# Kernel optimization log

Hardware: AMD Instinct MI355X
Metric: run time of the kernel (lower is better)

The kernel has to match this reference:

```python
import jax, jax.numpy as jnp
import numpy as np

SIGMA = 1.0  # kernel bandwidth (init kwarg)

VS = 4096   # src vertices
VT = 4096   # tar vertices
FS = 8192   # src triangles
FT = 8192   # tar triangles
FR = 8192   # reference triangles


def setup_inputs() -> dict:
    key = jax.random.key(0)
    k0, k1, k2, k3, k4, k5 = jax.random.split(key, 6)
    src_vertices = jax.random.normal(k0, (VS, 3), dtype=jnp.float32)
    src_indices = jax.random.randint(k1, (FS, 3), 0, VS, dtype=jnp.int64)
    tar_vertices = jax.random.normal(k2, (VT, 3), dtype=jnp.float32)
    tar_indices = jax.random.randint(k3, (FT, 3), 0, VT, dtype=jnp.int64)
    ref_normals = 0.1 * jax.random.normal(k4, (FR, 3), dtype=jnp.float32)
    ref_centers = jax.random.normal(k5, (FR, 3), dtype=jnp.float32)
    return {
        "src_vertices": src_vertices,
        "src_indices": src_indices,
        "tar_vertices": tar_vertices,
        "tar_indices": tar_indices,
        "ref_normals": ref_normals,
        "ref_centers": ref_centers,
    }


def _tri_normals_centers(vertices, indices):
    tris = vertices[indices]               # [F, 3, 3]
    a, b, c = tris[:, 0, :], tris[:, 1, :], tris[:, 2, :]
    normals = 0.5 * jnp.cross(a - b, c - b)  # [F, 3]
    centers = tris.sum(axis=1) / 3.0         # [F, 3]
    return normals, centers


def _sqdist(src, tar):
    # d[i, j] = ||tar_i - src_j||^2  -> shape [Nt, Ns]
    s2 = jnp.sum(src * src, axis=-1)  # [Ns]
    t2 = jnp.sum(tar * tar, axis=-1)  # [Nt]
    return t2[:, None] + s2[None, :] - 2.0 * (tar @ src.T)


def _cauchy(d):
    return 1.0 / (1.0 + d / SIGMA) ** 2


def _energy(sn, sc, tn, tc):
    e1 = jnp.sum((sn @ sn.T) * _cauchy(_sqdist(sc, sc)))
    e2 = jnp.sum((tn @ sn.T) * _cauchy(_sqdist(sc, tc)))
    e3 = jnp.sum((tn @ tn.T) * _cauchy(_sqdist(tc, tc)))
    return e1 - 2.0 * e2 + e3


def reference(src_vertices, src_indices, tar_vertices, tar_indices, ref_normals, ref_centers):
    src_n, src_c = _tri_normals_centers(src_vertices, src_indices)
    tar_n, tar_c = _tri_normals_centers(tar_vertices, tar_indices)
    energy = _energy(src_n, src_c, ref_normals, ref_centers)
    energy = energy + _energy(tar_n, tar_c, ref_normals, ref_centers)
    energy = energy + 0.8 * _energy(src_n, src_c, tar_n, tar_c)
    return energy
```

## Files before the change

kernel.cpp:

```cpp
#include <hip/hip_runtime.h>

#define NSEG 8192
#define NPTS (3 * NSEG)
#define NSUP 96
#define NXB  192
#define NYG  13

typedef short bf16x8 __attribute__((ext_vector_type(8)));
typedef float f32x16 __attribute__((ext_vector_type(16)));
typedef unsigned short u16;

__device__ __forceinline__ u16 f2bf(float x) {
    unsigned u = __builtin_bit_cast(unsigned, x);
    return (u16)((u + 0x7FFFu + ((u >> 16) & 1u)) >> 16);
}
__device__ __forceinline__ float bf2f(u16 h) {
    unsigned u = ((unsigned)h) << 16;
    return __builtin_bit_cast(float, u);
}

__device__ __forceinline__ void compute_point(
    int seg, int f,
    const float* __restrict__ sv, const int* __restrict__ si,
    const float* __restrict__ tv, const int* __restrict__ ti,
    const float* __restrict__ rn, const float* __restrict__ rc,
    float& cx, float& cy, float& cz, float& nx, float& ny, float& nz)
{
    if (seg == 2) {
        nx = rn[3*f];   ny = rn[3*f+1]; nz = rn[3*f+2];
        cx = rc[3*f];   cy = rc[3*f+1]; cz = rc[3*f+2];
    } else {
        const float* v  = (seg == 0) ? sv : tv;
        const int*   nd = (seg == 0) ? si : ti;
        int i0 = nd[3*f], i1 = nd[3*f+1], i2 = nd[3*f+2];
        float ax = v[3*i0], ay = v[3*i0+1], az = v[3*i0+2];
        float bx = v[3*i1], by = v[3*i1+1], bz = v[3*i1+2];
        float gx = v[3*i2], gy = v[3*i2+1], gz = v[3*i2+2];
        float ux = ax-bx, uy = ay-by, uz = az-bz;
        float wx = gx-bx, wy = gy-by, wz = gz-bz;
        nx = 0.5f*(uy*wz - uz*wy);
        ny = 0.5f*(uz*wx - ux*wz);
        nz = 0.5f*(ux*wy - uy*wx);
        cx = (ax+bx+gx)*(1.0f/3.0f);
        cy = (ay+by+gy)*(1.0f/3.0f);
        cz = (az+bz+gz)*(1.0f/3.0f);
    }
}

__global__ void setup_feats(const float* __restrict__ sv, const int* __restrict__ si,
                            const float* __restrict__ tv, const int* __restrict__ ti,
                            const float* __restrict__ rn, const float* __restrict__ rc,
                            u16* __restrict__ ws, float* __restrict__ out) {
    int gid = blockIdx.x * 256 + threadIdx.x;
    if (gid == 0) out[0] = 0.0f;
    const int rec = (gid >= NPTS);
    const int p   = rec ? gid - NPTS : gid;
    int seg = p >> 13, f = p & (NSEG - 1);
    float cx, cy, cz, nx, ny, nz;
    compute_point(seg, f, sv, si, tv, ti, rn, rc, cx, cy, cz, nx, ny, nz);

    const u16 ONE = 0x3F80;
    float s = cx*cx + cy*cy + cz*cz;
    u16 chx = f2bf(cx), chy = f2bf(cy), chz = f2bf(cz);
    u16 clx = f2bf(cx - bf2f(chx)), cly = f2bf(cy - bf2f(chy)), clz = f2bf(cz - bf2f(chz));
    u16 sh  = f2bf(s);
    u16 sl  = f2bf(s - bf2f(sh));
    u16 nhx = f2bf(nx), nhy = f2bf(ny), nhz = f2bf(nz);
    u16 nlx = f2bf(nx - bf2f(nhx)), nly = f2bf(ny - bf2f(nhy)), nlz = f2bf(nz - bf2f(nhz));

    bf16x8* A8 = (bf16x8*)ws;
    bf16x8* B8 = A8 + (size_t)NPTS*4;
    u16 r0[16], r1[16];
    if (!rec) {
        u16 at[16] = {chx,chy,chz, clx,cly,clz, chx,chy,chz, sh, sl, ONE, ONE, ONE, 0, 0};
        u16 an[16] = {nhx,nhy,nhz, nlx,nly,nlz, nhx,nhy,nhz, 0,0,0,0,0,0,0};
        #pragma unroll
        for (int k = 0; k < 16; ++k) { r0[k] = at[k]; r1[k] = an[k]; }
    } else {
        u16 m2hx = f2bf(-2.0f*bf2f(chx)), m2hy = f2bf(-2.0f*bf2f(chy)), m2hz = f2bf(-2.0f*bf2f(chz));
        u16 m2lx = f2bf(-2.0f*bf2f(clx)), m2ly = f2bf(-2.0f*bf2f(cly)), m2lz = f2bf(-2.0f*bf2f(clz));
        u16 bt[16] = {m2hx,m2hy,m2hz, m2hx,m2hy,m2hz, m2lx,m2ly,m2lz, ONE, ONE, sh, sl, ONE, 0, 0};
        u16 bn[16] = {nhx,nhy,nhz, nhx,nhy,nhz, nlx,nly,nlz, 0,0,0,0,0,0,0};
        #pragma unroll
        for (int k = 0; k < 16; ++k) { r0[k] = bt[k]; r1[k] = bn[k]; }
    }
    bf16x8* dst = rec ? B8 : A8;
    bf16x8 v0, v1, v2, v3;
    #pragma unroll
    for (int k = 0; k < 8; ++k) { v0[k] = (short)r0[k]; v1[k] = (short)r0[k+8];
                                  v2[k] = (short)r1[k]; v3[k] = (short)r1[k+8]; }
    dst[(size_t)p*4+0] = v0; dst[(size_t)p*4+1] = v1;
    dst[(size_t)p*4+2] = v2; dst[(size_t)p*4+3] = v3;
}

__device__ __forceinline__ void mfma2_vgpr(const bf16x8& a1, const bf16x8& b1,
                                           const bf16x8& a2, const bf16x8& b2,
                                           const f32x16& Z, f32x16& d1, f32x16& d2) {
    asm("v_mfma_f32_32x32x16_bf16 %0, %2, %3, %6\n\t"
        "v_mfma_f32_32x32x16_bf16 %1, %4, %5, %6\n\t"
        "s_nop 7\n\t"
        "s_nop 7\n\t"
        "s_nop 7"
        : "=&v"(d1), "=&v"(d2)
        : "v"(a1), "v"(b1), "v"(a2), "v"(b2), "v"(Z));
}

__launch_bounds__(256, 3)
__global__ void energy_mfma(const u16* __restrict__ ws, float* __restrict__ out) {
    const int tid  = threadIdx.x;
    const int lane = tid & 63, wid = tid >> 6;
    const int half = lane >> 5, r32 = lane & 31;

    const int bx = blockIdx.x;
    const int X  = bx >> 1;
    const int g  = blockIdx.y;
    const int y0   = (g < 12) ? 4*g : 48;
    const int ycnt = (g < 12) ? 4 : 1;
    const int gi = X >> 5;

    const float Wt[9] = {1.8f, -0.8f, -1.0f,
                        -0.8f,  1.8f, -1.0f,
                        -1.0f, -1.0f,  2.0f};

    const bf16x8* A8 = (const bf16x8*)ws;
    const bf16x8* B8 = A8 + (size_t)NPTS*4;

    const int pi = X*256 + (bx & 1)*128 + wid*32 + r32;
    const bf16x8 at = A8[pi*4 + half];
    const bf16x8 an = A8[pi*4 + 2 + half];

    f32x16 Z;
    #pragma unroll
    for (int k = 0; k < 16; ++k) Z[k] = 0.0f;

    const int lofs = r32*4 + half;

    float acc = 0.0f;
    for (int yy = 0; yy < ycnt; ++yy) {
        const int y = y0 + yy;
        int J = X + y; if (J >= NSUP) J -= NSUP;
        const float mult = (y == 0 || y == 48) ? 1.0f : 2.0f;
        const float w = Wt[gi*3 + (J >> 5)] * mult;

        const int base = J*1024 + lofs;

        bf16x8 btf = B8[base];
        bf16x8 bnf = B8[base + 2];

        float ts0 = 0.0f, ts1 = 0.0f;
        #pragma unroll 2
        for (int jt = 0; jt < 8; ++jt) {
            int nofs = base + ((jt < 7) ? (jt + 1) : jt) * 128;
            bf16x8 nbt = B8[nofs];
            bf16x8 nbn = B8[nofs + 2];

            f32x16 ct, cn;
            mfma2_vgpr(at, btf, an, bnf, Z, ct, cn);

            #pragma unroll
            for (int gq = 0; gq < 4; ++gq) {
                float t0 = ct[4*gq+0], t1 = ct[4*gq+1], t2 = ct[4*gq+2], t3 = ct[4*gq+3];
                float q0 = t0*t0, q1 = t1*t1, q2 = t2*t2, q3 = t3*t3;
                float s01 = q0*q1, s23 = q2*q3;
                float r   = __builtin_amdgcn_rcpf(s01*s23);
                float u   = __builtin_fmaf(cn[4*gq+1], q0, cn[4*gq+0]*q1);
                float v   = __builtin_fmaf(cn[4*gq+3], q2, cn[4*gq+2]*q3);
                float num = __builtin_fmaf(v, s01, u*s23);
                if (gq & 1) ts1 = __builtin_fmaf(num, r, ts1);
                else        ts0 = __builtin_fmaf(num, r, ts0);
            }

            btf = nbt; bnf = nbn;
        }
        acc = __builtin_fmaf(w, ts0 + ts1, acc);
    }

    for (int off = 32; off; off >>= 1) acc += __shfl_down(acc, off, 64);
    __shared__ float partial[4];
    if ((tid & 63) == 0) partial[wid] = acc;
    __syncthreads();
    if (tid == 0)
        atomicAdd(out, (partial[0] + partial[1]) + (partial[2] + partial[3]));
}

extern "C" void kernel_launch(void* const* d_in, const int* in_sizes, int n_in,
                              void* d_out, int out_size, void* d_ws, size_t ws_size,
                              hipStream_t stream) {
    const float* sv = (const float*)d_in[0];
    const int*   si = (const int*)d_in[1];
    const float* tv = (const float*)d_in[2];
    const int*   ti = (const int*)d_in[3];
    const float* rn = (const float*)d_in[4];
    const float* rc = (const float*)d_in[5];
    float* out = (float*)d_out;
    u16*   ws  = (u16*)d_ws;

    setup_feats<<<2*NPTS/256, 256, 0, stream>>>(sv, si, tv, ti, rn, rc, ws, out);
    dim3 grid(NXB, NYG);
    energy_mfma<<<grid, 256, 0, stream>>>(ws, out);
}
```

Baseline: 119.5 us.

## Switch energy kernel to 16x16x32 MFMA tiles with zero-padded K lanes

Replaces the inline-asm 32x32x16 bf16 MFMA pair (with hard s_nop padding) with compiler builtins for 16x16x32 MFMA. Because K is only 16, the upper half of the K lanes read a zero vector stored in the workspace. Each block now covers 64 rows instead of 128, so the grid x dimension doubles, and launch bounds rise to 4 blocks per SIMD to improve occupancy. This removes the fixed nop stalls and shrinks the accumulator register footprint. In exchange, half of each MFMA's K work is wasted on zeros, and each B tile is reloaded by twice as many blocks.

Result: slower. 181.4 us (+51.8%).

```diff
diff --git a/kernel.cpp b/kernel.cpp
--- a/kernel.cpp
+++ b/kernel.cpp
@@ -3,11 +3,13 @@
 #define NSEG 8192
 #define NPTS (3 * NSEG)
 #define NSUP 96
-#define NXB  192
+#define NXB  384
 #define NYG  13
+#define NB4  (NPTS * 4)
+#define ZF   (NPTS * 8)
 
 typedef short bf16x8 __attribute__((ext_vector_type(8)));
-typedef float f32x16 __attribute__((ext_vector_type(16)));
+typedef float f32x4  __attribute__((ext_vector_type(4)));
 typedef unsigned short u16;
 
 __device__ __forceinline__ u16 f2bf(float x) {
@@ -52,7 +54,14 @@
                             const float* __restrict__ rn, const float* __restrict__ rc,
                             u16* __restrict__ ws, float* __restrict__ out) {
     int gid = blockIdx.x * 256 + threadIdx.x;
-    if (gid == 0) out[0] = 0.0f;
+    bf16x8* A8 = (bf16x8*)ws;
+    if (gid == 0) {
+        out[0] = 0.0f;
+        bf16x8 z;
+        #pragma unroll
+        for (int k = 0; k < 8; ++k) z[k] = 0;
+        A8[ZF] = z;
+    }
     const int rec = (gid >= NPTS);
     const int p   = rec ? gid - NPTS : gid;
     int seg = p >> 13, f = p & (NSEG - 1);
@@ -68,8 +77,7 @@
     u16 nhx = f2bf(nx), nhy = f2bf(ny), nhz = f2bf(nz);
     u16 nlx = f2bf(nx - bf2f(nhx)), nly = f2bf(ny - bf2f(nhy)), nlz = f2bf(nz - bf2f(nhz));
 
-    bf16x8* A8 = (bf16x8*)ws;
-    bf16x8* B8 = A8 + (size_t)NPTS*4;
+    bf16x8* B8 = A8 + NB4;
     u16 r0[16], r1[16];
     if (!rec) {
         u16 at[16] = {chx,chy,chz, clx,cly,clz, chx,chy,chz, sh, sl, ONE, ONE, ONE, 0, 0};
@@ -93,27 +101,17 @@
     dst[(size_t)p*4+2] = v2; dst[(size_t)p*4+3] = v3;
 }
 
-__device__ __forceinline__ void mfma2_vgpr(const bf16x8& a1, const bf16x8& b1,
-                                           const bf16x8& a2, const bf16x8& b2,
-                                           const f32x16& Z, f32x16& d1, f32x16& d2) {
-    asm("v_mfma_f32_32x32x16_bf16 %0, %2, %3, %6\n\t"
-        "v_mfma_f32_32x32x16_bf16 %1, %4, %5, %6\n\t"
-        "s_nop 7\n\t"
-        "s_nop 7\n\t"
-        "s_nop 7"
-        : "=&v"(d1), "=&v"(d2)
-        : "v"(a1), "v"(b1), "v"(a2), "v"(b2), "v"(Z));
-}
-
-__launch_bounds__(256, 3)
+__launch_bounds__(256, 4)
 __global__ void energy_mfma(const u16* __restrict__ ws, float* __restrict__ out) {
     const int tid  = threadIdx.x;
     const int lane = tid & 63, wid = tid >> 6;
-    const int half = lane >> 5, r32 = lane & 31;
+    const int n16  = lane & 15, q = lane >> 4;
+    const bool lo2 = (q < 2);
 
-    const int bx = blockIdx.x;
-    const int X  = bx >> 1;
-    const int g  = blockIdx.y;
+    const int bx  = blockIdx.x;
+    const int X   = bx >> 2;
+    const int sub = bx & 3;
+    const int g   = blockIdx.y;
     const int y0   = (g < 12) ? 4*g : 48;
     const int ycnt = (g < 12) ? 4 : 1;
     const int gi = X >> 5;
@@ -122,18 +120,14 @@
                         -0.8f,  1.8f, -1.0f,
                         -1.0f, -1.0f,  2.0f};
 
-    const bf16x8* A8 = (const bf16x8*)ws;
-    const bf16x8* B8 = A8 + (size_t)NPTS*4;
+    const bf16x8* W8 = (const bf16x8*)ws;
 
-    const int pi = X*256 + (bx & 1)*128 + wid*32 + r32;
-    const bf16x8 at = A8[pi*4 + half];
-    const bf16x8 an = A8[pi*4 + 2 + half];
+    const int pi = X*256 + sub*64 + wid*16 + n16;
+    const bf16x8 at = W8[lo2 ? pi*4 + q     : ZF];
+    const bf16x8 an = W8[lo2 ? pi*4 + 2 + q : ZF];
 
-    f32x16 Z;
-    #pragma unroll
-    for (int k = 0; k < 16; ++k) Z[k] = 0.0f;
-
-    const int lofs = r32*4 + half;
+    f32x4 Z = {0.0f, 0.0f, 0.0f, 0.0f};
+    const int lofs = n16*4 + q;
 
     float acc = 0.0f;
     for (int yy = 0; yy < ycnt; ++yy) {
@@ -142,33 +136,30 @@
         const float mult = (y == 0 || y == 48) ? 1.0f : 2.0f;
         const float w = Wt[gi*3 + (J >> 5)] * mult;
 
-        const int base = J*1024 + lofs;
+        const int Jbase = NB4 + J*1024;
 
-        bf16x8 btf = B8[base];
-        bf16x8 bnf = B8[base + 2];
+        bf16x8 btf = W8[lo2 ? Jbase + lofs     : ZF];
+        bf16x8 bnf = W8[lo2 ? Jbase + lofs + 2 : ZF];
 
         float ts0 = 0.0f, ts1 = 0.0f;
-        #pragma unroll 2
-        for (int jt = 0; jt < 8; ++jt) {
-            int nofs = base + ((jt < 7) ? (jt + 1) : jt) * 128;
-            bf16x8 nbt = B8[nofs];
-            bf16x8 nbn = B8[nofs + 2];
+        #pragma unroll 4
+        for (int jt = 0; jt < 16; ++jt) {
+            int jn = Jbase + ((jt < 15) ? (jt + 1) : jt) * 64;
+            bf16x8 nbt = W8[lo2 ? jn + lofs     : ZF];
+            bf16x8 nbn = W8[lo2 ? jn + lofs + 2 : ZF];
 
-            f32x16 ct, cn;
-            mfma2_vgpr(at, btf, an, bnf, Z, ct, cn);
+            f32x4 ct = __builtin_amdgcn_mfma_f32_16x16x32_bf16(at, btf, Z, 0, 0, 0);
+            f32x4 cn = __builtin_amdgcn_mfma_f32_16x16x32_bf16(an, bnf, Z, 0, 0, 0);
 
-            #pragma unroll
-            for (int gq = 0; gq < 4; ++gq) {
-                float t0 = ct[4*gq+0], t1 = ct[4*gq+1], t2 = ct[4*gq+2], t3 = ct[4*gq+3];
-                float q0 = t0*t0, q1 = t1*t1, q2 = t2*t2, q3 = t3*t3;
-                float s01 = q0*q1, s23 = q2*q3;
-                float r   = __builtin_amdgcn_rcpf(s01*s23);
-                float u   = __builtin_fmaf(cn[4*gq+1], q0, cn[4*gq+0]*q1);
-                float v   = __builtin_fmaf(cn[4*gq+3], q2, cn[4*gq+2]*q3);
-                float num = __builtin_fmaf(v, s01, u*s23);
-                if (gq & 1) ts1 = __builtin_fmaf(num, r, ts1);
-                else        ts0 = __builtin_fmaf(num, r, ts0);
-            }
+            float q0 = ct[0]*ct[0], q1 = ct[1]*ct[1];
+            float q2 = ct[2]*ct[2], q3 = ct[3]*ct[3];
+            float s01 = q0*q1, s23 = q2*q3;
+            float r   = __builtin_amdgcn_rcpf(s01*s23);
+            float u   = __builtin_fmaf(cn[1], q0, cn[0]*q1);
+            float v   = __builtin_fmaf(cn[3], q2, cn[2]*q3);
+            float num = __builtin_fmaf(v, s01, u*s23);
+            if (jt & 1) ts1 = __builtin_fmaf(num, r, ts1);
+            else        ts0 = __builtin_fmaf(num, r, ts0);
 
             btf = nbt; bnf = nbn;
         }
```
